# Kernel optimization log

Measured on AMD Instinct MI355X. Metric: run time of the kernel, lower is better.

Reference implementation:

```python
import jax, jax.numpy as jnp
import numpy as np

EPS = 1e-5


def causal_conv(x, w, b):
    # x: [B,C,N,T], w: [O,C,K] (temporal kernel), b: [O]; left-pad time by K-1 (causal)
    K = w.shape[-1]
    y = jax.lax.conv_general_dilated(
        x, w[:, :, None, :], window_strides=(1, 1),
        padding=[(0, 0), (K - 1, 0)],
        dimension_numbers=('NCHW', 'OIHW', 'NCHW'))
    return y + b[None, :, None, None]


def batchnorm(x, gamma, beta):
    # training-mode BatchNorm2d: stats over (B, N, T) per channel
    m = x.mean(axis=(0, 2, 3), keepdims=True)
    v = x.var(axis=(0, 2, 3), keepdims=True)
    return (x - m) * jax.lax.rsqrt(v + EPS) * gamma[None, :, None, None] + beta[None, :, None, None]


def st_layer(x, supports, gamma, beta, rw, rb, aw, ab, gw, gb, ow, ob):
    # residual 1x1 conv
    res = jnp.einsum('bcnt,oc->bont', x, rw) + rb[None, :, None, None]
    x = jax.nn.relu(batchnorm(x, gamma, beta))
    aff = causal_conv(x, aw, ab)
    gate = causal_conv(x, gw, gb)
    x = jnp.tanh(aff + res) * jax.nn.sigmoid(gate)
    B, C, N, T = x.shape
    hs = jnp.einsum('bcvt,evw->becwt', x, supports)  # [B,E,C,N,T]
    full = jnp.concatenate([x, hs.reshape(B, -1, N, T)], axis=1)  # [B,C*(E+1),N,T]
    return jnp.einsum('bcnt,oc->bont', full, ow) + ob[None, :, None, None]


def reference(x, supports, bn_gamma, bn_beta, res_w, res_b, aff_w, aff_b,
              gate_w, gate_b, gc_w, gc_b, attn_w1, attn_b1, attn_w2, attn_b2,
              attn_w3, attn_b3):
    L = bn_gamma.shape[0]
    h = x
    stack = [x]
    for i in range(L):
        h = st_layer(h, supports, bn_gamma[i], bn_beta[i], res_w[i], res_b[i],
                     aff_w[i], aff_b[i], gate_w[i], gate_b[i], gc_w[i], gc_b[i])
        stack.append(h)
    xs = jax.nn.relu(jnp.stack(stack, axis=2))  # [B,C,L+1,N,T]
    # SelfAttention: 1x1x1 conv3d chain C->64->64->1 with ReLU after first two
    e = jax.nn.relu(jnp.einsum('bclnt,oc->bolnt', xs, attn_w1) + attn_b1[None, :, None, None, None])
    e = jax.nn.relu(jnp.einsum('bclnt,oc->bolnt', e, attn_w2) + attn_b2[None, :, None, None, None])
    e = jnp.einsum('bclnt,oc->bolnt', e, attn_w3) + attn_b3[None, :, None, None, None]  # [B,1,L+1,N,T]
    w = jax.nn.softmax(e, axis=2)
    out = (xs * w).sum(axis=2)  # [B,C,N,T]
    return out


def setup_inputs() -> dict:
    B, C, N, T = 16, 32, 500, 64
    L, E, K, D = 4, 2, 3, 64
    key = jax.random.key(0)
    ks = jax.random.split(key, 20)
    s = 0.1
    return {
        'x': jax.random.normal(ks[0], (B, C, N, T), jnp.float32),
        'supports': jax.random.uniform(ks[1], (E, N, N), jnp.float32) / N,
        'bn_gamma': jnp.ones((L, C), jnp.float32),
        'bn_beta': jnp.zeros((L, C), jnp.float32),
        'res_w': jax.random.normal(ks[2], (L, C, C), jnp.float32) * s,
        'res_b': jax.random.normal(ks[3], (L, C), jnp.float32) * s,
        'aff_w': jax.random.normal(ks[4], (L, C, C, K), jnp.float32) * s,
        'aff_b': jax.random.normal(ks[5], (L, C), jnp.float32) * s,
        'gate_w': jax.random.normal(ks[6], (L, C, C, K), jnp.float32) * s,
        'gate_b': jax.random.normal(ks[7], (L, C), jnp.float32) * s,
        'gc_w': jax.random.normal(ks[8], (L, C, C * (E + 1)), jnp.float32) * s,
        'gc_b': jax.random.normal(ks[9], (L, C), jnp.float32) * s,
        'attn_w1': jax.random.normal(ks[10], (D, C), jnp.float32) * s,
        'attn_b1': jax.random.normal(ks[11], (D,), jnp.float32) * s,
        'attn_w2': jax.random.normal(ks[12], (D, D), jnp.float32) * s,
        'attn_b2': jax.random.normal(ks[13], (D,), jnp.float32) * s,
        'attn_w3': jax.random.normal(ks[14], (1, D), jnp.float32) * s,
        'attn_b3': jax.random.normal(ks[15], (1,), jnp.float32) * s,
    }
```

## Files before the change

kernel.cpp:

```cpp
#include <hip/hip_runtime.h>
#include <hip/hip_bf16.h>
#include <math.h>

#define B_ 16
#define C_ 32
#define N_ 500
#define T_ 64
#define L_ 4
#define BSTR (C_*N_*T_)
#define CSTR (N_*T_)
#define TENS ((size_t)B_*C_*N_*T_)
#define CNT_ 512000.0

typedef short s8v __attribute__((ext_vector_type(8)));
typedef float f4v __attribute__((ext_vector_type(4)));
typedef unsigned short u16;

__global__ __launch_bounds__(256) void zero_kernel(double* __restrict__ p) {
  p[threadIdx.x] = 0.0;
}

__global__ __launch_bounds__(256) void stats_kernel(const float* __restrict__ h,
                                                    double* __restrict__ st) {
  int c = blockIdx.x, b = blockIdx.y, tid = threadIdx.x;
  const float4* p = (const float4*)(h + (size_t)b*BSTR + (size_t)c*CSTR);
  double s = 0.0, s2 = 0.0;
  for (int i = tid; i < CSTR/4; i += 256) {
    float4 v = p[i];
    s  += (double)v.x + (double)v.y + (double)v.z + (double)v.w;
    s2 += (double)v.x*v.x + (double)v.y*v.y + (double)v.z*v.z + (double)v.w*v.w;
  }
  __shared__ double sd[256], sd2[256];
  sd[tid] = s; sd2[tid] = s2; __syncthreads();
  for (int off = 128; off > 0; off >>= 1) {
    if (tid < off) { sd[tid] += sd[tid+off]; sd2[tid] += sd2[tid+off]; }
    __syncthreads();
  }
  if (tid == 0) { atomicAdd(&st[2*c], sd[0]); atomicAdd(&st[2*c+1], sd2[0]); }
}

__global__ __launch_bounds__(256) void aconv_kernel(const float* __restrict__ sup,
                                                    short* __restrict__ ATh,
                                                    short* __restrict__ ATl) {
  int idx = blockIdx.x*256 + threadIdx.x;
  int k = idx & 1023, w = idx >> 10;
  int s = k >> 9, v = k & 511;
  float val = (v < N_ && w < N_) ? sup[((size_t)s*N_ + v)*N_ + w] : 0.f;
  __hip_bfloat16 bh = __float2bfloat16(val);
  float fh = __bfloat162float(bh);
  __hip_bfloat16 bl = __float2bfloat16(val - fh);
  ATh[idx] = *(short*)&bh;
  ATl[idx] = *(short*)&bl;
}

__global__ __launch_bounds__(256) void w1t_kernel(const float* __restrict__ W1,
                                                  float* __restrict__ W1T) {
  int idx = blockIdx.x*256 + threadIdx.x;
  int c = idx >> 6, k = idx & 63;
  W1T[c*64 + k] = W1[k*32 + c];
}

__global__ __launch_bounds__(256) void wprep_kernel(
    const float* __restrict__ aw, const float* __restrict__ gw,
    const float* __restrict__ rw,
    u16* __restrict__ wagh, u16* __restrict__ wagl,
    u16* __restrict__ wrh,  u16* __restrict__ wrl)
{
  int idx = blockIdx.x*256 + threadIdx.x;
  if (idx >= 28672) return;
  float v; u16 *dh, *dl; int di;
  if (idx < 24576) {
    int l = idx / 6144, r = idx % 6144;
    int tap = r / 2048, col = (r >> 5) & 63, c = r & 31;
    v = (col < 32) ? aw[l*3072 + (col*32 + c)*3 + tap]
                   : gw[l*3072 + ((col-32)*32 + c)*3 + tap];
    dh = wagh; dl = wagl; di = idx;
  } else {
    int j = idx - 24576;
    int l = j >> 10, o = (j >> 5) & 31, c = j & 31;
    v = rw[l*1024 + o*32 + c];
    dh = wrh; dl = wrl; di = j;
  }
  __hip_bfloat16 bh = __float2bfloat16(v);
  float fh = __bfloat162float(bh);
  __hip_bfloat16 bl = __float2bfloat16(v - fh);
  dh[di] = *(u16*)&bh;
  dl[di] = *(u16*)&bl;
}

__global__ __launch_bounds__(512) void fuse4_kernel(
    const float* __restrict__ h, const double* __restrict__ st,
    const float* __restrict__ gamma, const float* __restrict__ beta,
    const u16* __restrict__ wagh, const u16* __restrict__ wagl,
    const u16* __restrict__ wrh,  const u16* __restrict__ wrl,
    const float* __restrict__ rb, const float* __restrict__ ab,
    const float* __restrict__ gb,
    const float* __restrict__ gcw, const float* __restrict__ gcb,
    float* __restrict__ Y0, u16* __restrict__ Y1h, u16* __restrict__ Y2h)
{
  __shared__ __align__(16) char smem[41600];
  __shared__ float ssc[C_], ssb[C_];
  u16* Sxh = (u16*)smem;
  u16* Sxl = Sxh + 5280;
  u16* Shh = Sxl + 5280;
  u16* Shl = Shh + 5120;
  float* Sz = (float*)smem;

  int tid = threadIdx.x;
  int bx  = blockIdx.x;
  int b = bx / 250, np = bx - b*250;
  size_t off0 = (size_t)b*BSTR + (size_t)(np*2)*T_;

  int m  = tid & 127;
  int c0 = (tid >> 7) << 3;
  float hv[8];
  #pragma unroll
  for (int j = 0; j < 8; j++)
    hv[j] = h[off0 + (size_t)(c0 + j)*CSTR + m];

  if (tid < C_) {
    double mm = st[2*tid] * (1.0/CNT_);
    double vv = st[2*tid+1] * (1.0/CNT_) - mm*mm;
    float sc = gamma[tid] * (float)(1.0 / sqrt(vv + 1e-5));
    ssc[tid] = sc;
    ssb[tid] = beta[tid] - (float)mm * sc;
  }
  __syncthreads();

  union P { u16 s[8]; int4 v; };
  P hh8, hl8, xh8, xl8;
  #pragma unroll
  for (int j = 0; j < 8; j++) {
    float hval = hv[j];
    __hip_bfloat16 t1 = __float2bfloat16(hval);
    hh8.s[j] = *(u16*)&t1;
    __hip_bfloat16 t2 = __float2bfloat16(hval - __bfloat162float(t1));
    hl8.s[j] = *(u16*)&t2;
    float xval = fmaxf(fmaf(hval, ssc[c0+j], ssb[c0+j]), 0.f);
    __hip_bfloat16 t3 = __float2bfloat16(xval);
    xh8.s[j] = *(u16*)&t3;
    __hip_bfloat16 t4 = __float2bfloat16(xval - __bfloat162float(t3));
    xl8.s[j] = *(u16*)&t4;
  }
  *(int4*)&Shh[m*40 + c0] = hh8.v;
  *(int4*)&Shl[m*40 + c0] = hl8.v;
  int xrow = m + 2 + (m >> 6)*2;
  *(int4*)&Sxh[xrow*40 + c0] = xh8.v;
  *(int4*)&Sxl[xrow*40 + c0] = xl8.v;
  if (tid < 32) {
    int pl = tid >> 4, rsel = (tid >> 2) & 3, ch = tid & 3;
    int row = (rsel & 1) + (rsel >> 1)*66;
    int4 z4 = {0,0,0,0};
    *(int4*)((pl ? Sxl : Sxh) + row*40 + ch*8) = z4;
  }
  __syncthreads();

  int lane = tid & 63;
  int wave = __builtin_amdgcn_readfirstlane(tid >> 6);
  int node = wave >> 2, t0 = (wave & 3) << 4;
  int l15 = lane & 15, q = lane >> 4;

  f4v affc[2], gatec[2], resc[2];
  #pragma unroll
  for (int i = 0; i < 2; i++) {
    affc[i] = (f4v){0.f,0.f,0.f,0.f};
    gatec[i] = (f4v){0.f,0.f,0.f,0.f};
    resc[i] = (f4v){0.f,0.f,0.f,0.f};
  }

  {
    int ha = (node*64 + t0 + l15)*40 + q*8;
    s8v hhf = *(const s8v*)&Shh[ha];
    s8v hlf = *(const s8v*)&Shl[ha];
    #pragma unroll
    for (int ct = 0; ct < 2; ct++) {
      int wb = (ct*16 + l15)*32 + q*8;
      s8v wh = *(const s8v*)&wrh[wb];
      s8v wl = *(const s8v*)&wrl[wb];
      f4v d = resc[ct];
      d = __builtin_amdgcn_mfma_f32_16x16x32_bf16(hhf, wh, d, 0, 0, 0);
      d = __builtin_amdgcn_mfma_f32_16x16x32_bf16(hlf, wh, d, 0, 0, 0);
      d = __builtin_amdgcn_mfma_f32_16x16x32_bf16(hhf, wl, d, 0, 0, 0);
      resc[ct] = d;
    }
  }
  #pragma unroll
  for (int tap = 0; tap < 3; tap++) {
    int xa = (node*66 + t0 + l15 + tap)*40 + q*8;
    s8v xhf = *(const s8v*)&Sxh[xa];
    s8v xlf = *(const s8v*)&Sxl[xa];
    #pragma unroll
    for (int ct = 0; ct < 4; ct++) {
      int wb = (tap*64 + ct*16 + l15)*32 + q*8;
      s8v wh = *(const s8v*)&wagh[wb];
      s8v wl = *(const s8v*)&wagl[wb];
      f4v d = (ct < 2) ? affc[ct] : gatec[ct-2];
      d = __builtin_amdgcn_mfma_f32_16x16x32_bf16(xhf, wh, d, 0, 0, 0);
      d = __builtin_amdgcn_mfma_f32_16x16x32_bf16(xlf, wh, d, 0, 0, 0);
      d = __builtin_amdgcn_mfma_f32_16x16x32_bf16(xhf, wl, d, 0, 0, 0);
      if (ct < 2) affc[ct] = d; else gatec[ct-2] = d;
    }
  }
  __syncthreads();

  #pragma unroll
  for (int ct = 0; ct < 2; ct++) {
    int o = ct*16 + l15;
    float abias = ab[o] + rb[o];
    float gbias = gb[o];
    #pragma unroll
    for (int r = 0; r < 4; r++) {
      float a = affc[ct][r] + resc[ct][r] + abias;
      float g = gatec[ct][r] + gbias;
      float z = tanhf(a) * (1.f/(1.f + expf(-g)));
      Sz[node*2080 + o*65 + (t0 + q*4 + r)] = z;
    }
  }
  __syncthreads();

  int t = tid & 63;
  int og = wave;
  float y0a[2][4] = {}, y1a[2][4] = {}, y2a[2][4] = {};
  for (int c = 0; c < C_; c++) {
    float g0[4], g1[4], g2[4];
    #pragma unroll
    for (int jq = 0; jq < 4; jq++) {
      const float* gr = gcw + (og*4 + jq)*96;
      g0[jq] = gr[c]; g1[jq] = gr[32 + c]; g2[jq] = gr[64 + c];
    }
    #pragma unroll
    for (int nn = 0; nn < 2; nn++) {
      float zc = Sz[nn*2080 + c*65 + t];
      #pragma unroll
      for (int jq = 0; jq < 4; jq++) {
        y0a[nn][jq] = fmaf(g0[jq], zc, y0a[nn][jq]);
        y1a[nn][jq] = fmaf(g1[jq], zc, y1a[nn][jq]);
        y2a[nn][jq] = fmaf(g2[jq], zc, y2a[nn][jq]);
      }
    }
  }
  #pragma unroll
  for (int nn = 0; nn < 2; nn++)
    #pragma unroll
    for (int jq = 0; jq < 4; jq++) {
      int oo = og*4 + jq;
      size_t pp = off0 + (size_t)nn*T_ + (size_t)oo*CSTR + t;
      Y0[pp] = y0a[nn][jq] + gcb[oo];
      __hip_bfloat16 b1 = __float2bfloat16(y1a[nn][jq]);
      __hip_bfloat16 b2 = __float2bfloat16(y2a[nn][jq]);
      Y1h[pp] = *(u16*)&b1;
      Y2h[pp] = *(u16*)&b2;
    }
}

__global__ __launch_bounds__(256) void diff3_kernel(
    const u16* __restrict__ Y1h, const u16* __restrict__ Y2h,
    const short* __restrict__ ATh, const short* __restrict__ ATl,
    float* __restrict__ out, double* __restrict__ stp)
{
  __shared__ short Asd[2][64*40];
  __shared__ short Bsd[128*40];

  int tid = threadIdx.x;
  int bx = blockIdx.x;
  int mtile = bx & 15, wtile = bx >> 4;
  int b = blockIdx.y;
  int w0 = wtile << 6;

  int lane = tid & 63;
  int wave = __builtin_amdgcn_readfirstlane(tid >> 6);
  int wi = wave & 1, wj = wave >> 1;
  int l15 = lane & 15, quad = lane >> 4;

  int offA[2], offB[4];
  #pragma unroll
  for (int ti = 0; ti < 2; ti++) offA[ti] = (wi*32 + ti*16 + l15)*40 + quad*8;
  #pragma unroll
  for (int tj = 0; tj < 4; tj++) offB[tj] = (wj*64 + tj*16 + l15)*40 + quad*8;

  f4v acc[8];
  #pragma unroll
  for (int i = 0; i < 8; i++) acc[i] = (f4v){0.f, 0.f, 0.f, 0.f};

  int t_l = tid & 63;
  int g = tid >> 6;

  for (int k0 = 0; k0 < 1024; k0 += 32) {
    __syncthreads();
    #pragma unroll
    for (int i = 0; i < 2; i++) {
      int idx = tid + i*256;
      int kq = idx & 3, wl = (idx >> 2) & 63, pl = idx >> 8;
      const short* sp = (pl ? ATl : ATh) + (size_t)(w0 + wl)*1024 + k0 + kq*8;
      int4 v = *(const int4*)sp;
      *(int4*)&Asd[pl][wl*40 + kq*8] = v;
    }
    {
      int s  = k0 >> 9;
      int v0 = k0 & 511;
      const u16* Ys = (s ? Y2h : Y1h) + (size_t)b*BSTR;
      #pragma unroll
      for (int i = 0; i < 2; i++) {
        int sel = g*2 + i;
        int oo = sel & 1, kq = sel >> 1;
        int o = mtile*2 + oo;
        u16 hs[8];
        #pragma unroll
        for (int j = 0; j < 8; j++) {
          int v = v0 + kq*8 + j;
          hs[j] = (v < N_) ? Ys[((size_t)o*N_ + v)*T_ + t_l] : (u16)0;
        }
        *(int4*)&Bsd[(oo*64 + t_l)*40 + kq*8] = *(const int4*)hs;
      }
    }
    __syncthreads();
    s8v bh[4];
    #pragma unroll
    for (int tj = 0; tj < 4; tj++) bh[tj] = *(const s8v*)&Bsd[offB[tj]];
    #pragma unroll
    for (int ti = 0; ti < 2; ti++) {
      s8v ah = *(const s8v*)&Asd[0][offA[ti]];
      s8v al = *(const s8v*)&Asd[1][offA[ti]];
      #pragma unroll
      for (int tj = 0; tj < 4; tj++) {
        f4v d = acc[ti*4+tj];
        d = __builtin_amdgcn_mfma_f32_16x16x32_bf16(ah, bh[tj], d, 0, 0, 0);
        d = __builtin_amdgcn_mfma_f32_16x16x32_bf16(al, bh[tj], d, 0, 0, 0);
        acc[ti*4+tj] = d;
      }
    }
  }

  int o = mtile*2 + wj;
  float s = 0.f, s2 = 0.f;
  #pragma unroll
  for (int tj = 0; tj < 4; tj++) {
    int t = tj*16 + l15;
    float* obase = out + (((size_t)b*C_ + o)*N_)*T_ + t;
    #pragma unroll
    for (int ti = 0; ti < 2; ti++) {
      int wbase = w0 + wi*32 + ti*16 + quad*4;
      #pragma unroll
      for (int r = 0; r < 4; r++) {
        int w = wbase + r;
        if (w < N_) {
          float* p = obase + (size_t)w*T_;
          float val = *p + acc[ti*4+tj][r];
          *p = val;
          s += val;
          s2 = fmaf(val, val, s2);
        }
      }
    }
  }
  if (stp) {
    #pragma unroll
    for (int d = 32; d > 0; d >>= 1) {
      s  += __shfl_down(s,  d, 64);
      s2 += __shfl_down(s2, d, 64);
    }
    if (lane == 0) {
      atomicAdd(&stp[2*o],     (double)s);
      atomicAdd(&stp[2*o + 1], (double)s2);
    }
  }
}

__global__ __launch_bounds__(256) void attn3_kernel(
    const float* __restrict__ hsrc, float* __restrict__ O,
    float* __restrict__ sden,
    const float* __restrict__ W1T, const float* __restrict__ b1,
    const float* __restrict__ W2, const float* __restrict__ b2,
    const float* __restrict__ w3, const float* __restrict__ b3,
    int init)
{
  int tid = threadIdx.x;
  int t = tid & 63;
  int g = __builtin_amdgcn_readfirstlane(tid >> 6);
  int bx = blockIdx.x;
  int b = bx / 125;
  int n = (bx - b*125)*4 + g;
  size_t off = (size_t)b*BSTR + (size_t)n*T_;

  float h1r[64];
  #pragma unroll
  for (int k = 0; k < 64; k++) h1r[k] = b1[k];
  for (int c = 0; c < C_; c++) {
    float xv = fmaxf(hsrc[off + (size_t)c*CSTR + t], 0.f);
    const float* wr = W1T + c*64;
    #pragma unroll
    for (int k = 0; k < 64; k++) h1r[k] = fmaf(wr[k], xv, h1r[k]);
  }
  #pragma unroll
  for (int k = 0; k < 64; k++) h1r[k] = fmaxf(h1r[k], 0.f);

  float e = b3[0];
  for (int j = 0; j < 64; j++) {
    const float* w2r = W2 + j*64;
    float a0 = 0.f, a1 = 0.f, a2 = 0.f, a3 = 0.f;
    #pragma unroll
    for (int i = 0; i < 64; i += 4) {
      a0 = fmaf(w2r[i+0], h1r[i+0], a0);
      a1 = fmaf(w2r[i+1], h1r[i+1], a1);
      a2 = fmaf(w2r[i+2], h1r[i+2], a2);
      a3 = fmaf(w2r[i+3], h1r[i+3], a3);
    }
    float a = b2[j] + ((a0+a1)+(a2+a3));
    e = fmaf(w3[j], fmaxf(a, 0.f), e);
  }
  float p = expf(e);

  size_t si = (size_t)b*CSTR + (size_t)n*T_ + t;
  float so = init ? 0.f : sden[si];
  sden[si] = so + p;

  for (int c = 0; c < C_; c++) {
    size_t pi = off + (size_t)c*CSTR + t;
    float xv = fmaxf(hsrc[pi], 0.f);
    float ov = init ? 0.f : O[pi];
    O[pi] = fmaf(p, xv, ov);
  }
}

__global__ __launch_bounds__(256) void norm_kernel(float* __restrict__ O,
                                                   const float* __restrict__ sden) {
  unsigned idx = (blockIdx.x*256u + threadIdx.x) * 4u;
  unsigned b = idx / BSTR;
  unsigned r = idx - b*BSTR;
  unsigned nt = r % CSTR;
  float4 o = *(float4*)(O + idx);
  const float* sp = sden + (size_t)b*CSTR + nt;
  o.x /= sp[0]; o.y /= sp[1]; o.z /= sp[2]; o.w /= sp[3];
  *(float4*)(O + idx) = o;
}

extern "C" void kernel_launch(void* const* d_in, const int* in_sizes, int n_in,
                              void* d_out, int out_size, void* d_ws, size_t ws_size,
                              hipStream_t stream)
{
  const float* x    = (const float*)d_in[0];
  const float* sup  = (const float*)d_in[1];
  const float* bng  = (const float*)d_in[2];
  const float* bnb  = (const float*)d_in[3];
  const float* rw   = (const float*)d_in[4];
  const float* rb   = (const float*)d_in[5];
  const float* aw   = (const float*)d_in[6];
  const float* ab   = (const float*)d_in[7];
  const float* gw   = (const float*)d_in[8];
  const float* gb   = (const float*)d_in[9];
  const float* gcw  = (const float*)d_in[10];
  const float* gcb  = (const float*)d_in[11];
  const float* w1   = (const float*)d_in[12];
  const float* ab1  = (const float*)d_in[13];
  const float* w2   = (const float*)d_in[14];
  const float* ab2  = (const float*)d_in[15];
  const float* w3   = (const float*)d_in[16];
  const float* ab3  = (const float*)d_in[17];
  float* out = (float*)d_out;

  float* ws   = (float*)d_ws;
  float* bufA = ws;
  u16*   Y1h  = (u16*)(ws + TENS);
  u16*   Y2h  = Y1h + TENS;
  float* sden = ws + (size_t)3*TENS;
  double* st  = (double*)(ws + (size_t)3*TENS + (size_t)B_*N_*T_);
  short* ATh  = (short*)(ws + (size_t)3*TENS + (size_t)B_*N_*T_ + 512);
  short* ATl  = ATh + (size_t)512*1024;
  float* W1T  = (float*)(ATl + (size_t)512*1024);
  u16* WAGh = (u16*)(W1T + 2048);
  u16* WAGl = WAGh + 24576;
  u16* WRh  = WAGl + 24576;
  u16* WRl  = WRh + 4096;

  zero_kernel<<<1, 256, 0, stream>>>(st);
  aconv_kernel<<<2048, 256, 0, stream>>>(sup, ATh, ATl);
  w1t_kernel<<<8, 256, 0, stream>>>(w1, W1T);
  wprep_kernel<<<112, 256, 0, stream>>>(aw, gw, rw, WAGh, WAGl, WRh, WRl);
  stats_kernel<<<dim3(C_, B_), 256, 0, stream>>>(x, st);
  attn3_kernel<<<B_*125, 256, 0, stream>>>(x, out, sden, W1T, ab1, w2, ab2, w3, ab3, 1);

  const float* hcur = x;
  for (int l = 0; l < L_; l++) {
    fuse4_kernel<<<B_*250, 512, 0, stream>>>(
        hcur, st + l*64, bng + l*C_, bnb + l*C_,
        WAGh + l*6144, WAGl + l*6144, WRh + l*1024, WRl + l*1024,
        rb + l*C_, ab + l*C_, gb + l*C_,
        gcw + l*C_*96, gcb + l*C_,
        bufA, Y1h, Y2h);
    diff3_kernel<<<dim3(128, B_), 256, 0, stream>>>(
        Y1h, Y2h, ATh, ATl, bufA, (l < L_-1) ? (st + (l+1)*64) : nullptr);
    attn3_kernel<<<B_*125, 256, 0, stream>>>(bufA, out, sden, W1T, ab1, w2, ab2, w3, ab3, 0);
    hcur = bufA;
  }
  norm_kernel<<<16000, 256, 0, stream>>>(out, sden);
}
```

Before: 1.618 ms.

## Transpose diffusion operand in a separate pass, drop bf16 low split, register-pipeline MFMA

Adds a transpose kernel that lays Y1/Y2 out as [b,o,t,v] with the two supports packed contiguously along K. The graph-diffusion GEMM can then load MFMA fragments straight from global memory with double-buffered registers, with no LDS staging or barriers. The supports matrix is kept only as a single bf16 plane, which halves the MFMA work and the A traffic. In exchange there is an extra transpose launch with its own global round trip each layer, and the supports lose the precision the hi/lo split used to provide.

```diff
diff --git a/kernel.cpp b/kernel.cpp
--- a/kernel.cpp
+++ b/kernel.cpp
@@ -16,8 +16,10 @@
 typedef float f4v __attribute__((ext_vector_type(4)));
 typedef unsigned short u16;
 
-__global__ __launch_bounds__(256) void zero_kernel(double* __restrict__ p) {
+__global__ __launch_bounds__(256) void zero_kernel(double* __restrict__ p,
+                                                   float* __restrict__ slack) {
   p[threadIdx.x] = 0.0;
+  if (threadIdx.x < 16) slack[threadIdx.x] = 0.f;
 }
 
 __global__ __launch_bounds__(256) void stats_kernel(const float* __restrict__ h,
@@ -40,17 +42,17 @@
 }
 
 __global__ __launch_bounds__(256) void aconv_kernel(const float* __restrict__ sup,
-                                                    short* __restrict__ ATh,
-                                                    short* __restrict__ ATl) {
+                                                    short* __restrict__ ATh) {
   int idx = blockIdx.x*256 + threadIdx.x;
   int k = idx & 1023, w = idx >> 10;
-  int s = k >> 9, v = k & 511;
-  float val = (v < N_ && w < N_) ? sup[((size_t)s*N_ + v)*N_ + w] : 0.f;
+  float val = 0.f;
+  if (k < 1000 && w < N_) {
+    int s = k >= 500;
+    int v = k - s*500;
+    val = sup[((size_t)s*N_ + v)*N_ + w];
+  }
   __hip_bfloat16 bh = __float2bfloat16(val);
-  float fh = __bfloat162float(bh);
-  __hip_bfloat16 bl = __float2bfloat16(val - fh);
   ATh[idx] = *(short*)&bh;
-  ATl[idx] = *(short*)&bl;
 }
 
 __global__ __launch_bounds__(256) void w1t_kernel(const float* __restrict__ W1,
@@ -253,14 +255,55 @@
     }
 }
 
-__global__ __launch_bounds__(256) void diff3_kernel(
+__global__ __launch_bounds__(256) void trans_kernel(
     const u16* __restrict__ Y1h, const u16* __restrict__ Y2h,
-    const short* __restrict__ ATh, const short* __restrict__ ATl,
+    u16* __restrict__ Yt)
+{
+  __shared__ u16 S[64*68];
+  int bx = blockIdx.x;
+  int o = bx & 31, vg = bx >> 5;
+  int b = blockIdx.y;
+  int tid = threadIdx.x;
+  u16* dst = Yt + (size_t)(b*C_ + o)*64000;
+  for (int ic = 0; ic < 4; ic++) {
+    int vc = vg*4 + ic;
+    __syncthreads();
+    #pragma unroll
+    for (int i = 0; i < 2; i++) {
+      int vrow = (tid >> 3) + i*32;
+      int vv = vc*64 + vrow;
+      int t8 = (tid & 7)*8;
+      int4 val = {0,0,0,0};
+      if (vv < 1000) {
+        int sup = vv >= 500;
+        int n = vv - sup*500;
+        const u16* src = (sup ? Y2h : Y1h) + (size_t)b*BSTR + (size_t)o*CSTR
+                         + (size_t)n*T_;
+        val = *(const int4*)(src + t8);
+      }
+      *(int4*)&S[vrow*68 + t8] = val;
+    }
+    __syncthreads();
+    int t2 = tid >> 3, vs = tid & 7;
+    if (vc < 15 || vs < 5) {
+      unsigned r[8];
+      #pragma unroll
+      for (int j = 0; j < 8; j++)
+        r[j] = *(const unsigned*)&S[(vs*8 + j)*68 + 2*t2];
+      u16 lo[8], hi[8];
+      #pragma unroll
+      for (int j = 0; j < 8; j++) { lo[j] = (u16)r[j]; hi[j] = (u16)(r[j] >> 16); }
+      *(int4*)(dst + (size_t)(2*t2)*1000   + vc*64 + vs*8) = *(const int4*)lo;
+      *(int4*)(dst + (size_t)(2*t2+1)*1000 + vc*64 + vs*8) = *(const int4*)hi;
+    }
+  }
+}
+
+__global__ __launch_bounds__(256) void diff4_kernel(
+    const u16* __restrict__ Yt,
+    const short* __restrict__ ATh,
     float* __restrict__ out, double* __restrict__ stp)
 {
-  __shared__ short Asd[2][64*40];
-  __shared__ short Bsd[128*40];
-
   int tid = threadIdx.x;
   int bx = blockIdx.x;
   int mtile = bx & 15, wtile = bx >> 4;
@@ -271,67 +314,46 @@
   int wave = __builtin_amdgcn_readfirstlane(tid >> 6);
   int wi = wave & 1, wj = wave >> 1;
   int l15 = lane & 15, quad = lane >> 4;
-
-  int offA[2], offB[4];
-  #pragma unroll
-  for (int ti = 0; ti < 2; ti++) offA[ti] = (wi*32 + ti*16 + l15)*40 + quad*8;
-  #pragma unroll
-  for (int tj = 0; tj < 4; tj++) offB[tj] = (wj*64 + tj*16 + l15)*40 + quad*8;
+  int o = mtile*2 + wj;
+
+  const short* pA[2]; const u16* pB[4];
+  #pragma unroll
+  for (int ti = 0; ti < 2; ti++)
+    pA[ti] = ATh + (size_t)(w0 + wi*32 + ti*16 + l15)*1024 + quad*8;
+  const u16* Ybase = Yt + (size_t)(b*C_ + o)*64000;
+  #pragma unroll
+  for (int tj = 0; tj < 4; tj++)
+    pB[tj] = Ybase + (size_t)(tj*16 + l15)*1000 + quad*8;
 
   f4v acc[8];
   #pragma unroll
   for (int i = 0; i < 8; i++) acc[i] = (f4v){0.f, 0.f, 0.f, 0.f};
 
-  int t_l = tid & 63;
-  int g = tid >> 6;
-
-  for (int k0 = 0; k0 < 1024; k0 += 32) {
-    __syncthreads();
-    #pragma unroll
-    for (int i = 0; i < 2; i++) {
-      int idx = tid + i*256;
-      int kq = idx & 3, wl = (idx >> 2) & 63, pl = idx >> 8;
-      const short* sp = (pl ? ATl : ATh) + (size_t)(w0 + wl)*1024 + k0 + kq*8;
-      int4 v = *(const int4*)sp;
-      *(int4*)&Asd[pl][wl*40 + kq*8] = v;
-    }
-    {
-      int s  = k0 >> 9;
-      int v0 = k0 & 511;
-      const u16* Ys = (s ? Y2h : Y1h) + (size_t)b*BSTR;
+  s8v a0[2], b0[4], a1[2], b1[4];
+
+  auto LOADS = [&](s8v (&av)[2], s8v (&bv)[4], int k0) {
+    #pragma unroll
+    for (int ti = 0; ti < 2; ti++) av[ti] = *(const s8v*)(pA[ti] + k0);
+    #pragma unroll
+    for (int tj = 0; tj < 4; tj++) bv[tj] = *(const s8v*)(pB[tj] + k0);
+  };
+  auto MM = [&](s8v (&av)[2], s8v (&bv)[4]) {
+    #pragma unroll
+    for (int ti = 0; ti < 2; ti++)
       #pragma unroll
-      for (int i = 0; i < 2; i++) {
-        int sel = g*2 + i;
-        int oo = sel & 1, kq = sel >> 1;
-        int o = mtile*2 + oo;
-        u16 hs[8];
-        #pragma unroll
-        for (int j = 0; j < 8; j++) {
-          int v = v0 + kq*8 + j;
-          hs[j] = (v < N_) ? Ys[((size_t)o*N_ + v)*T_ + t_l] : (u16)0;
-        }
-        *(int4*)&Bsd[(oo*64 + t_l)*40 + kq*8] = *(const int4*)hs;
-      }
-    }
-    __syncthreads();
-    s8v bh[4];
-    #pragma unroll
-    for (int tj = 0; tj < 4; tj++) bh[tj] = *(const s8v*)&Bsd[offB[tj]];
-    #pragma unroll
-    for (int ti = 0; ti < 2; ti++) {
-      s8v ah = *(const s8v*)&Asd[0][offA[ti]];
-      s8v al = *(const s8v*)&Asd[1][offA[ti]];
-      #pragma unroll
-      for (int tj = 0; tj < 4; tj++) {
-        f4v d = acc[ti*4+tj];
-        d = __builtin_amdgcn_mfma_f32_16x16x32_bf16(ah, bh[tj], d, 0, 0, 0);
-        d = __builtin_amdgcn_mfma_f32_16x16x32_bf16(al, bh[tj], d, 0, 0, 0);
-        acc[ti*4+tj] = d;
-      }
-    }
-  }
-
-  int o = mtile*2 + wj;
+      for (int tj = 0; tj < 4; tj++)
+        acc[ti*4+tj] = __builtin_amdgcn_mfma_f32_16x16x32_bf16(
+                           av[ti], bv[tj], acc[ti*4+tj], 0, 0, 0);
+  };
+
+  LOADS(a0, b0, 0);
+  for (int k0 = 0; k0 < 1024; k0 += 64) {
+    LOADS(a1, b1, k0 + 32);
+    MM(a0, b0);
+    if (k0 + 64 < 1024) LOADS(a0, b0, k0 + 64);
+    MM(a1, b1);
+  }
+
   float s = 0.f, s2 = 0.f;
   #pragma unroll
   for (int tj = 0; tj < 4; tj++) {
@@ -462,18 +484,19 @@
   float* bufA = ws;
   u16*   Y1h  = (u16*)(ws + TENS);
   u16*   Y2h  = Y1h + TENS;
-  float* sden = ws + (size_t)3*TENS;
-  double* st  = (double*)(ws + (size_t)3*TENS + (size_t)B_*N_*T_);
-  short* ATh  = (short*)(ws + (size_t)3*TENS + (size_t)B_*N_*T_ + 512);
-  short* ATl  = ATh + (size_t)512*1024;
-  float* W1T  = (float*)(ATl + (size_t)512*1024);
+  u16*   Yt   = (u16*)(ws + (size_t)2*TENS);
+  float* slack= ws + (size_t)2*TENS + 16384000;
+  float* sden = slack + 16;
+  double* st  = (double*)(sden + (size_t)B_*N_*T_);
+  short* ATh  = (short*)((float*)st + 1024);
+  float* W1T  = (float*)(ATh + (size_t)512*1024);
   u16* WAGh = (u16*)(W1T + 2048);
   u16* WAGl = WAGh + 24576;
   u16* WRh  = WAGl + 24576;
   u16* WRl  = WRh + 4096;
 
-  zero_kernel<<<1, 256, 0, stream>>>(st);
-  aconv_kernel<<<2048, 256, 0, stream>>>(sup, ATh, ATl);
+  zero_kernel<<<1, 256, 0, stream>>>(st, slack);
+  aconv_kernel<<<2048, 256, 0, stream>>>(sup, ATh);
   w1t_kernel<<<8, 256, 0, stream>>>(w1, W1T);
   wprep_kernel<<<112, 256, 0, stream>>>(aw, gw, rw, WAGh, WAGl, WRh, WRl);
   stats_kernel<<<dim3(C_, B_), 256, 0, stream>>>(x, st);
@@ -487,8 +510,9 @@
         rb + l*C_, ab + l*C_, gb + l*C_,
         gcw + l*C_*96, gcb + l*C_,
         bufA, Y1h, Y2h);
-    diff3_kernel<<<dim3(128, B_), 256, 0, stream>>>(
-        Y1h, Y2h, ATh, ATl, bufA, (l < L_-1) ? (st + (l+1)*64) : nullptr);
+    trans_kernel<<<dim3(128, B_), 256, 0, stream>>>(Y1h, Y2h, Yt);
+    diff4_kernel<<<dim3(128, B_), 256, 0, stream>>>(
+        Yt, ATh, bufA, (l < L_-1) ? (st + (l+1)*64) : nullptr);
     attn3_kernel<<<B_*125, 256, 0, stream>>>(bufA, out, sden, W1T, ab1, w2, ab2, w3, ab3, 0);
     hcur = bufA;
   }
```

Result: slower. 1.713 ms (+5.9%).
